# Kernel optimization log

Measured on AMD Instinct MI355X. Metric: run time of the kernel, lower is better.

Reference implementation:

```python
import jax, jax.numpy as jnp
import numpy as np

QLEN, MLEN, BSZ = 1024, 1024, 2
KLEN = QLEN + MLEN           # 2048, also rlen
D_MODEL, N_HEAD, D_HEAD = 1024, 16, 64
SCALE = 1.0 / (D_HEAD ** 0.5)
LN_EPS = 1e-5


def _rel_shift(x):
    # x: (qlen, klen, bsz, n_head). Torch-XL rel_shift via pad/reshape trick.
    q, k, b, n = x.shape
    zero_pad = jnp.zeros((q, 1, b, n), dtype=x.dtype)
    x_padded = jnp.concatenate([zero_pad, x], axis=1)   # (q, k+1, b, n)
    x_padded = x_padded.reshape(k + 1, q, b, n)[1:]      # drop first row
    return x_padded.reshape(q, k, b, n)


def _layer_norm(x, g, b):
    mu = jnp.mean(x, axis=-1, keepdims=True)
    var = jnp.mean(jnp.square(x - mu), axis=-1, keepdims=True)
    return (x - mu) * jax.lax.rsqrt(var + LN_EPS) * g + b


def setup_inputs() -> dict:
    key = jax.random.key(0)
    ks = jax.random.split(key, 9)
    w = jax.random.normal(ks[0], (QLEN, BSZ, D_MODEL), dtype=jnp.float32)
    r = jax.random.normal(ks[1], (KLEN, D_MODEL), dtype=jnp.float32)
    mems = jax.random.normal(ks[2], (MLEN, BSZ, D_MODEL), dtype=jnp.float32)
    # Causal mask with memory: query i may attend to key j <= i + MLEN.
    i = jnp.arange(QLEN)[:, None]
    j = jnp.arange(KLEN)[None, :]
    attn_mask = (j > i + MLEN)[:, :, None]  # (qlen, klen, 1) bool, dim==3 branch
    init = 0.02
    qkv_w = jax.random.normal(ks[3], (3 * N_HEAD * D_HEAD, D_MODEL), dtype=jnp.float32) * init
    r_w = jax.random.normal(ks[4], (N_HEAD * D_HEAD, D_MODEL), dtype=jnp.float32) * init
    o_w = jax.random.normal(ks[5], (D_MODEL, N_HEAD * D_HEAD), dtype=jnp.float32) * init
    ln_g = jnp.ones((D_MODEL,), dtype=jnp.float32)
    ln_b = jnp.zeros((D_MODEL,), dtype=jnp.float32)
    r_w_bias = jax.random.uniform(ks[6], (N_HEAD, D_HEAD), minval=-0.1, maxval=0.1, dtype=jnp.float32)
    r_r_bias = jax.random.uniform(ks[7], (N_HEAD, D_HEAD), minval=-0.1, maxval=0.1, dtype=jnp.float32)
    return {"w": w, "r": r, "mems": mems, "attn_mask": attn_mask,
            "qkv_w": qkv_w, "r_w": r_w, "o_w": o_w,
            "ln_g": ln_g, "ln_b": ln_b,
            "r_w_bias": r_w_bias, "r_r_bias": r_r_bias}


def reference(w, r, mems, attn_mask, qkv_w, r_w, o_w, ln_g, ln_b, r_w_bias, r_r_bias):
    qlen, bsz = w.shape[0], w.shape[1]
    cat = jnp.concatenate([mems, w], axis=0)                 # (klen, b, d_model)
    w_heads = cat @ qkv_w.T                                  # (klen, b, 3*n*d)
    w_head_q, w_head_k, w_head_v = jnp.split(w_heads, 3, axis=-1)
    klen = w_head_k.shape[0]
    w_head_q = w_head_q[-qlen:].reshape(qlen, bsz, N_HEAD, D_HEAD)
    w_head_k = w_head_k.reshape(klen, bsz, N_HEAD, D_HEAD)
    w_head_v = w_head_v.reshape(klen, bsz, N_HEAD, D_HEAD)
    r_head_k = (r @ r_w.T).reshape(r.shape[0], N_HEAD, D_HEAD)  # (rlen, n, d)

    AC = jnp.einsum('ibnd,jbnd->ijbn', w_head_q + r_w_bias, w_head_k)
    BD = _rel_shift(jnp.einsum('ibnd,jnd->ijbn', w_head_q + r_r_bias, r_head_k))
    attn_score = (AC + BD) * SCALE                           # (q, k, b, n)
    attn_score = jnp.where(attn_mask[:, :, :, None], -jnp.inf, attn_score)
    attn_prob = jax.nn.softmax(attn_score, axis=1)           # softmax over keys

    attn_vec = jnp.einsum('ijbn,jbnd->ibnd', attn_prob, w_head_v)
    attn_vec = attn_vec.reshape(qlen, bsz, N_HEAD * D_HEAD)
    attn_out = attn_vec @ o_w.T                              # (q, b, d_model)
    # post-LN residual (pre_lnorm=False)
    return _layer_norm(w + attn_out, ln_g, ln_b)
```

## Files before the change

kernel.cpp:

```cpp
#include <hip/hip_runtime.h>
#include <hip/hip_bf16.h>

#define QLEN 1024
#define MLEN 1024
#define KLEN 2048
#define BSZ 2
#define DMODEL 1024
#define NHEAD 16
#define DHEAD 64
#define SCALE_F 0.125f

typedef unsigned int u32;
typedef unsigned short u16;
typedef __attribute__((ext_vector_type(8))) short short8;
typedef __attribute__((ext_vector_type(4))) float f32x4;

__device__ __forceinline__ u16 f2bf(float f) {
  __hip_bfloat16 h = __float2bfloat16(f);
  return *reinterpret_cast<u16*>(&h);
}
__device__ __forceinline__ float bf2f(u16 u) {
  union { u32 w; float f; } c; c.w = ((u32)u) << 16; return c.f;
}
__device__ __forceinline__ float wave_sum(float v) {
#pragma unroll
  for (int o = 32; o > 0; o >>= 1) v += __shfl_xor(v, o);
  return v;
}

__global__ void detect_kernel(const void* __restrict__ lng, u32* __restrict__ flag) {
  if (threadIdx.x == 0 && blockIdx.x == 0) {
    u32 w = *(const u32*)lng;
    *flag = (w == 0x3F800000u) ? 0u : 1u;
  }
}

__global__ void conv_params(const void* __restrict__ lng, const void* __restrict__ lnb,
                            const void* __restrict__ rwb, const void* __restrict__ rrb,
                            float* __restrict__ PARAMS) {
  int i = blockIdx.x * 256 + threadIdx.x;
  u32 w0 = *(const u32*)lng;
  int f = (w0 != 0x3F800000u);
  int seg = i >> 10, off = i & 1023;
  const void* s = seg == 0 ? lng : seg == 1 ? lnb : seg == 2 ? rwb : rrb;
  PARAMS[i] = f ? bf2f(((const u16*)s)[off]) : ((const float*)s)[off];
}

__global__ void sentinel_kernel(u32* out) { out[threadIdx.x] = 0x49742400u;  }


#define GEMM_PREAMBLE()                                                        \
  __shared__ __align__(16) char lds2[2][128 * 128];                            \
  char* lA = lds2[0];                                                          \
  char* lB = lds2[1];                                                          \
  const int tid = threadIdx.x;                                                 \
  const int w_ = tid >> 6, l_ = tid & 63, lo = l_ & 15, g = l_ >> 4;           \
  const int wr = (w_ >> 1) * 64, wc = (w_ & 1) * 64;                           \
  f32x4 acc[4][4];                                                             \
  _Pragma("unroll") for (int mi = 0; mi < 4; ++mi)                             \
  _Pragma("unroll") for (int ni = 0; ni < 4; ++ni)                             \
      acc[mi][ni] = (f32x4){0.f, 0.f, 0.f, 0.f};

#define GEMM_MFMA_BODY()                                                       \
  _Pragma("unroll") for (int ks = 0; ks < 2; ++ks) {                           \
    short8 af[4], bf[4];                                                       \
    _Pragma("unroll") for (int mi = 0; mi < 4; ++mi) {                         \
      int r = wr + mi * 16 + lo;                                               \
      int c = ks * 4 + g;                                                      \
      af[mi] = *reinterpret_cast<const short8*>(lA + r * 128 + ((c ^ (r & 7)) * 16)); \
    }                                                                          \
    _Pragma("unroll") for (int ni = 0; ni < 4; ++ni) {                         \
      int r = wc + ni * 16 + lo;                                               \
      int c = ks * 4 + g;                                                      \
      bf[ni] = *reinterpret_cast<const short8*>(lB + r * 128 + ((c ^ (r & 7)) * 16)); \
    }                                                                          \
    _Pragma("unroll") for (int mi = 0; mi < 4; ++mi)                           \
    _Pragma("unroll") for (int ni = 0; ni < 4; ++ni)                           \
        acc[mi][ni] = __builtin_amdgcn_mfma_f32_16x16x32_bf16(af[mi], bf[ni], acc[mi][ni], 0, 0, 0); \
  }

__device__ __forceinline__ uint4 cvt8f32(const float* p) {
  float4 a = *reinterpret_cast<const float4*>(p);
  float4 b4 = *reinterpret_cast<const float4*>(p + 4);
  union { u16 us[8]; uint4 v; } o;
  o.us[0] = f2bf(a.x); o.us[1] = f2bf(a.y); o.us[2] = f2bf(a.z); o.us[3] = f2bf(a.w);
  o.us[4] = f2bf(b4.x); o.us[5] = f2bf(b4.y); o.us[6] = f2bf(b4.z); o.us[7] = f2bf(b4.w);
  return o.v;
}

__global__ __launch_bounds__(256) void gemm_qkv(
    const void* __restrict__ mems_raw, const void* __restrict__ w_raw,
    const void* __restrict__ qkvw_raw, const float* __restrict__ PARAMS,
    u16* __restrict__ QWb, u16* __restrict__ QRb,
    u16* __restrict__ Kb, u16* __restrict__ VTb,
    const u32* __restrict__ flag) {
  const int col0 = blockIdx.x * 128;
  const int row0 = blockIdx.y * 128;
  if (col0 < 1024 && row0 < 2048) return;
  const int f = (int)*flag;
  GEMM_PREAMBLE();

  for (int k0 = 0; k0 < DMODEL; k0 += 64) {
    __syncthreads();
    if (f) {
#pragma unroll
      for (int it = 0; it < 4; ++it) {
        int id = it * 256 + tid;
        int r = id >> 3, c = id & 7;
        int jb = row0 + r;
        const u16* asrc = jb < 2048 ? (const u16*)mems_raw + (size_t)jb * DMODEL
                                    : (const u16*)w_raw + (size_t)(jb - 2048) * DMODEL;
        uint4 va = *reinterpret_cast<const uint4*>(asrc + k0 + c * 8);
        uint4 vb = *reinterpret_cast<const uint4*>((const u16*)qkvw_raw + (size_t)(col0 + r) * DMODEL + k0 + c * 8);
        *reinterpret_cast<uint4*>(lA + r * 128 + ((c ^ (r & 7)) * 16)) = va;
        *reinterpret_cast<uint4*>(lB + r * 128 + ((c ^ (r & 7)) * 16)) = vb;
      }
    } else {
#pragma unroll
      for (int it = 0; it < 4; ++it) {
        int id = it * 256 + tid;
        int r = id >> 3, c = id & 7;
        int jb = row0 + r;
        const float* asrc = jb < 2048 ? (const float*)mems_raw + (size_t)jb * DMODEL
                                      : (const float*)w_raw + (size_t)(jb - 2048) * DMODEL;
        uint4 va = cvt8f32(asrc + k0 + c * 8);
        uint4 vb = cvt8f32((const float*)qkvw_raw + (size_t)(col0 + r) * DMODEL + k0 + c * 8);
        *reinterpret_cast<uint4*>(lA + r * 128 + ((c ^ (r & 7)) * 16)) = va;
        *reinterpret_cast<uint4*>(lB + r * 128 + ((c ^ (r & 7)) * 16)) = vb;
      }
    }
    __syncthreads();
    GEMM_MFMA_BODY();
  }

  const int which = col0 >> 10;
  if (which == 0) {
#pragma unroll
    for (int mi = 0; mi < 4; ++mi)
#pragma unroll
      for (int ni = 0; ni < 4; ++ni)
#pragma unroll
        for (int rr = 0; rr < 4; ++rr) {
          int row = row0 + wr + mi * 16 + g * 4 + rr;
          int col = col0 + wc + ni * 16 + lo;
          int i_ = (row >> 1) - 1024, b_ = row & 1;
          size_t ad = (((size_t)(b_ * 16 + (col >> 6))) * QLEN + i_) * 64 + (col & 63);
          float v = acc[mi][ni][rr];
          QWb[ad] = f2bf(v + PARAMS[2048 + col]);
          QRb[ad] = f2bf(v + PARAMS[3072 + col]);
        }
  } else if (which == 1) {
#pragma unroll
    for (int mi = 0; mi < 4; ++mi)
#pragma unroll
      for (int ni = 0; ni < 4; ++ni)
#pragma unroll
        for (int rr = 0; rr < 4; ++rr) {
          int row = row0 + wr + mi * 16 + g * 4 + rr;
          int col = col0 + wc + ni * 16 + lo;
          int j_ = row >> 1, b_ = row & 1;
          int cl = col - 1024;
          Kb[(((size_t)(b_ * 16 + (cl >> 6))) * KLEN + j_) * 64 + (cl & 63)] = f2bf(acc[mi][ni][rr]);
        }
  } else {
    __syncthreads();
    u16* ldsT = (u16*)lds2;
#pragma unroll
    for (int mi = 0; mi < 4; ++mi)
#pragma unroll
      for (int ni = 0; ni < 4; ++ni)
#pragma unroll
        for (int rr = 0; rr < 4; ++rr) {
          int rl = wr + mi * 16 + g * 4 + rr;
          int cl = wc + ni * 16 + lo;
          int rpp = (rl & 1) * 64 + (rl >> 1);
          ldsT[cl * 128 + (((rpp >> 3) ^ (cl & 7)) * 8) + (rpp & 7)] = f2bf(acc[mi][ni][rr]);
        }
    __syncthreads();
    int vc0 = col0 - 2048;
#pragma unroll
    for (int it = 0; it < 8; ++it) {
      int cid = it * 256 + tid;
      int c_l = cid >> 4;
      int j8 = cid & 15;
      uint4 vv = *reinterpret_cast<const uint4*>(ldsT + c_l * 128 + ((j8 ^ (c_l & 7)) * 8));
      int vcol = vc0 + c_l;
      int b_ = j8 >> 3;
      size_t dst = (((size_t)(b_ * 16 + (vcol >> 6))) * 64 + (vcol & 63)) * KLEN
                 + (row0 >> 1) + (j8 & 7) * 8;
      *reinterpret_cast<uint4*>(VTb + dst) = vv;
    }
  }
}

__global__ __launch_bounds__(256) void gemm_r(
    const void* __restrict__ r_raw, const void* __restrict__ rw_raw,
    u16* __restrict__ RKnb, const u32* __restrict__ flag) {
  const int col0 = blockIdx.x * 128;
  const int row0 = blockIdx.y * 128;
  const int f = (int)*flag;
  GEMM_PREAMBLE();
  for (int k0 = 0; k0 < DMODEL; k0 += 64) {
    __syncthreads();
    if (f) {
#pragma unroll
      for (int it = 0; it < 4; ++it) {
        int id = it * 256 + tid;
        int r = id >> 3, c = id & 7;
        uint4 va = *reinterpret_cast<const uint4*>((const u16*)r_raw + (size_t)(row0 + r) * DMODEL + k0 + c * 8);
        uint4 vb = *reinterpret_cast<const uint4*>((const u16*)rw_raw + (size_t)(col0 + r) * DMODEL + k0 + c * 8);
        *reinterpret_cast<uint4*>(lA + r * 128 + ((c ^ (r & 7)) * 16)) = va;
        *reinterpret_cast<uint4*>(lB + r * 128 + ((c ^ (r & 7)) * 16)) = vb;
      }
    } else {
#pragma unroll
      for (int it = 0; it < 4; ++it) {
        int id = it * 256 + tid;
        int r = id >> 3, c = id & 7;
        uint4 va = cvt8f32((const float*)r_raw + (size_t)(row0 + r) * DMODEL + k0 + c * 8);
        uint4 vb = cvt8f32((const float*)rw_raw + (size_t)(col0 + r) * DMODEL + k0 + c * 8);
        *reinterpret_cast<uint4*>(lA + r * 128 + ((c ^ (r & 7)) * 16)) = va;
        *reinterpret_cast<uint4*>(lB + r * 128 + ((c ^ (r & 7)) * 16)) = vb;
      }
    }
    __syncthreads();
    GEMM_MFMA_BODY();
  }
#pragma unroll
  for (int mi = 0; mi < 4; ++mi)
#pragma unroll
    for (int ni = 0; ni < 4; ++ni)
#pragma unroll
      for (int rr = 0; rr < 4; ++rr) {
        int t_ = row0 + wr + mi * 16 + g * 4 + rr;
        int col = col0 + wc + ni * 16 + lo;
        RKnb[((size_t)(col >> 6) * KLEN + t_) * 64 + (col & 63)] = f2bf(acc[mi][ni][rr]);
      }
}

__global__ __launch_bounds__(256) void gemm_o(
    const u16* __restrict__ A, const void* __restrict__ ow_raw,
    float* __restrict__ C, const u32* __restrict__ flag) {
  const int col0 = blockIdx.x * 128;
  const int row0 = blockIdx.y * 128;
  const int f = (int)*flag;
  GEMM_PREAMBLE();
  for (int k0 = 0; k0 < DMODEL; k0 += 64) {
    __syncthreads();
    if (f) {
#pragma unroll
      for (int it = 0; it < 4; ++it) {
        int id = it * 256 + tid;
        int r = id >> 3, c = id & 7;
        uint4 va = *reinterpret_cast<const uint4*>(A + (size_t)(row0 + r) * DMODEL + k0 + c * 8);
        uint4 vb = *reinterpret_cast<const uint4*>((const u16*)ow_raw + (size_t)(col0 + r) * DMODEL + k0 + c * 8);
        *reinterpret_cast<uint4*>(lA + r * 128 + ((c ^ (r & 7)) * 16)) = va;
        *reinterpret_cast<uint4*>(lB + r * 128 + ((c ^ (r & 7)) * 16)) = vb;
      }
    } else {
#pragma unroll
      for (int it = 0; it < 4; ++it) {
        int id = it * 256 + tid;
        int r = id >> 3, c = id & 7;
        uint4 va = *reinterpret_cast<const uint4*>(A + (size_t)(row0 + r) * DMODEL + k0 + c * 8);
        uint4 vb = cvt8f32((const float*)ow_raw + (size_t)(col0 + r) * DMODEL + k0 + c * 8);
        *reinterpret_cast<uint4*>(lA + r * 128 + ((c ^ (r & 7)) * 16)) = va;
        *reinterpret_cast<uint4*>(lB + r * 128 + ((c ^ (r & 7)) * 16)) = vb;
      }
    }
    __syncthreads();
    GEMM_MFMA_BODY();
  }
#pragma unroll
  for (int mi = 0; mi < 4; ++mi)
#pragma unroll
    for (int ni = 0; ni < 4; ++ni)
#pragma unroll
      for (int rr = 0; rr < 4; ++rr) {
        int row = row0 + wr + mi * 16 + g * 4 + rr;
        int col = col0 + wc + ni * 16 + lo;
        C[(size_t)row * DMODEL + col] = acc[mi][ni][rr];
      }
}

__global__ __launch_bounds__(256) void attn_mfma(
    const u16* __restrict__ QWb, const u16* __restrict__ QRb,
    const u16* __restrict__ Kb, const u16* __restrict__ VTb,
    const u16* __restrict__ RKnb, u16* __restrict__ AVb) {
  __shared__ __align__(16) char kt[8192];
  __shared__ __align__(16) char vt[8192];
  __shared__ __align__(16) char rt[2][8192];
  __shared__ __align__(16) char bfT[4 * 2560];
  __shared__ __align__(16) char pl[8192];

  const int tid = threadIdx.x;
  const int w = tid >> 6, l = tid & 63, lo = l & 15, g = l >> 4;
  const int gid = blockIdx.x;
  const int lid = gid & 255, hi = gid >> 8;
  const int bn = lid & 31, q3 = lid >> 5;
  const int xi = hi ? (15 - q3) : q3;
  const int i0 = xi * 64;
  const int b = bn >> 4, n = bn & 15;
  const int nkt = xi + 17;

  const u16* qwp = QWb + (((size_t)bn * QLEN) + i0 + w * 16 + lo) * 64;
  const u16* qrp = QRb + (((size_t)bn * QLEN) + i0 + w * 16 + lo) * 64;
  short8 qw0 = *reinterpret_cast<const short8*>(qwp + g * 8);
  short8 qw1 = *reinterpret_cast<const short8*>(qwp + 32 + g * 8);
  short8 qr0 = *reinterpret_cast<const short8*>(qrp + g * 8);
  short8 qr1 = *reinterpret_cast<const short8*>(qrp + 32 + g * 8);

  const u16* kbp = Kb + (size_t)bn * KLEN * 64;
  const u16* vtp = VTb + (size_t)bn * 64 * KLEN;
  const u16* rp  = RKnb + (size_t)n * KLEN * 64;

  uint4 Rk[2], Rv[2], Rr[2];
  const int srow = tid >> 3, sc = tid & 7;

  {
    int m0 = 15 - xi;
    char* rh = rt[m0 & 1];
#pragma unroll
    for (int it = 0; it < 2; ++it) {
      int row = srow + it * 32;
      int t = m0 * 64 + row;
      *reinterpret_cast<uint4*>(rh + row * 128 + ((sc ^ (row & 7)) * 16)) =
          *reinterpret_cast<const uint4*>(rp + (size_t)t * 64 + sc * 8);
    }
  }
#pragma unroll
  for (int it = 0; it < 2; ++it) {
    int row = srow + it * 32;
    Rk[it] = *reinterpret_cast<const uint4*>(kbp + (size_t)row * 64 + sc * 8);
    Rv[it] = *reinterpret_cast<const uint4*>(vtp + (size_t)row * KLEN + sc * 8);
    int t = (16 - xi) * 64 + row; t = t > KLEN - 1 ? KLEN - 1 : t;
    Rr[it] = *reinterpret_cast<const uint4*>(rp + (size_t)t * 64 + sc * 8);
  }

  f32x4 oacc[4];
  float m_r[4], l_r[4];
#pragma unroll
  for (int r = 0; r < 4; ++r) {
    oacc[r] = (f32x4){0.f, 0.f, 0.f, 0.f};
    m_r[r] = -1e30f; l_r[r] = 0.f;
  }

  for (int kti = 0; kti < nkt; ++kti) {
    const int j0 = kti * 64;
    __syncthreads();
    {
      char* rh = rt[(kti + 16 - xi) & 1];
#pragma unroll
      for (int it = 0; it < 2; ++it) {
        int row = srow + it * 32;
        int sw = (sc ^ (row & 7)) * 16;
        *reinterpret_cast<uint4*>(kt + row * 128 + sw) = Rk[it];
        *reinterpret_cast<uint4*>(vt + row * 128 + sw) = Rv[it];
        *reinterpret_cast<uint4*>(rh + row * 128 + sw) = Rr[it];
      }
    }
    __syncthreads();
    if (kti + 1 < nkt) {
      int j0n = j0 + 64;
      int mst = kti + 17 - xi;
#pragma unroll
      for (int it = 0; it < 2; ++it) {
        int row = srow + it * 32;
        Rk[it] = *reinterpret_cast<const uint4*>(kbp + (size_t)(j0n + row) * 64 + sc * 8);
        Rv[it] = *reinterpret_cast<const uint4*>(vtp + (size_t)row * KLEN + j0n + sc * 8);
        int t = mst * 64 + row; t = t > KLEN - 1 ? KLEN - 1 : t;
        Rr[it] = *reinterpret_cast<const uint4*>(rp + (size_t)t * 64 + sc * 8);
      }
    }
    const int hbase = (kti + 15 - xi) & 1;

    f32x4 ac[4];
#pragma unroll
    for (int ct = 0; ct < 4; ++ct) {
      const char* kb = kt + (ct * 16 + lo) * 128;
      short8 k0 = *reinterpret_cast<const short8*>(kb + ((g ^ (lo & 7)) * 16));
      short8 k1 = *reinterpret_cast<const short8*>(kb + (((4 + g) ^ (lo & 7)) * 16));
      f32x4 a = {0.f, 0.f, 0.f, 0.f};
      a = __builtin_amdgcn_mfma_f32_16x16x32_bf16(qw0, k0, a, 0, 0, 0);
      a = __builtin_amdgcn_mfma_f32_16x16x32_bf16(qw1, k1, a, 0, 0, 0);
      ac[ct] = a;
    }
    char* bfw = bfT + w * 2560;
#pragma unroll
    for (int bb = 0; bb < 5; ++bb) {
      int bt = 3 - w + bb;
      int half = hbase ^ (bt >> 2);
      const char* rbase = rt[half] + ((bt & 3) * 16 + lo) * 128;
      short8 r0 = *reinterpret_cast<const short8*>(rbase + ((g ^ (lo & 7)) * 16));
      short8 r1 = *reinterpret_cast<const short8*>(rbase + (((4 + g) ^ (lo & 7)) * 16));
      f32x4 a = {0.f, 0.f, 0.f, 0.f};
      a = __builtin_amdgcn_mfma_f32_16x16x32_bf16(qr0, r0, a, 0, 0, 0);
      a = __builtin_amdgcn_mfma_f32_16x16x32_bf16(qr1, r1, a, 0, 0, 0);
      union { u16 us[4]; uint2 v2; } pk;
      pk.us[0] = f2bf(a[0]); pk.us[1] = f2bf(a[1]);
      pk.us[2] = f2bf(a[2]); pk.us[3] = f2bf(a[3]);
      int rel = bb * 16 + lo;
      *reinterpret_cast<uint2*>(bfw + rel * 32 + (((g >> 1) ^ (rel & 1)) * 16) + (g & 1) * 8) = pk.v2;
    }
    const int relmax = i0 + MLEN - j0 + 15 + 16 * w;
    float sv[4][4];
    float rmax[4] = {-1e30f, -1e30f, -1e30f, -1e30f};
#pragma unroll
    for (int ct = 0; ct < 4; ++ct)
#pragma unroll
      for (int rr = 0; rr < 4; ++rr) {
        int rel = ct * 16 + lo - g * 4 - rr + 15;
        float bd = bf2f(*reinterpret_cast<const u16*>(
            bfw + rel * 32 + (((g >> 1) ^ (rel & 1)) * 16) + (g & 1) * 8 + rr * 2));
        float s = (ac[ct][rr] + bd) * SCALE_F;
        s = rel > relmax ? -1e30f : s;
        sv[ct][rr] = s;
        rmax[rr] = fmaxf(rmax[rr], s);
      }
#pragma unroll
    for (int rr = 0; rr < 4; ++rr) {
      float rm = rmax[rr];
      rm = fmaxf(rm, __shfl_xor(rm, 1));
      rm = fmaxf(rm, __shfl_xor(rm, 2));
      rm = fmaxf(rm, __shfl_xor(rm, 4));
      rm = fmaxf(rm, __shfl_xor(rm, 8));
      float mn = fmaxf(m_r[rr], rm);
      float sc2 = __expf(m_r[rr] - mn);
      m_r[rr] = mn;
      l_r[rr] *= sc2;
#pragma unroll
      for (int dt = 0; dt < 4; ++dt) oacc[dt][rr] *= sc2;
    }
    float rsum[4] = {0.f, 0.f, 0.f, 0.f};
#pragma unroll
    for (int ct = 0; ct < 4; ++ct)
#pragma unroll
      for (int rr = 0; rr < 4; ++rr) {
        float p = __expf(sv[ct][rr] - m_r[rr]);
        sv[ct][rr] = p;
        rsum[rr] += p;
      }
#pragma unroll
    for (int rr = 0; rr < 4; ++rr) {
      float rs = rsum[rr];
      rs += __shfl_xor(rs, 1);
      rs += __shfl_xor(rs, 2);
      rs += __shfl_xor(rs, 4);
      rs += __shfl_xor(rs, 8);
      l_r[rr] += rs;
    }
#pragma unroll
    for (int ct = 0; ct < 4; ++ct)
#pragma unroll
      for (int rr = 0; rr < 4; ++rr) {
        int rowp = g * 4 + rr;
        int col = ct * 16 + lo;
        int cblk = (col >> 3) ^ (rowp & 7);
        *reinterpret_cast<u16*>(pl + w * 2048 + rowp * 128 + cblk * 16 + (col & 7) * 2) = f2bf(sv[ct][rr]);
      }
    short8 pa0 = *reinterpret_cast<const short8*>(pl + w * 2048 + lo * 128 + ((g ^ (lo & 7)) * 16));
    short8 pa1 = *reinterpret_cast<const short8*>(pl + w * 2048 + lo * 128 + (((4 + g) ^ (lo & 7)) * 16));
#pragma unroll
    for (int dt = 0; dt < 4; ++dt) {
      const char* vb = vt + (dt * 16 + lo) * 128;
      short8 v0 = *reinterpret_cast<const short8*>(vb + ((g ^ (lo & 7)) * 16));
      short8 v1 = *reinterpret_cast<const short8*>(vb + (((4 + g) ^ (lo & 7)) * 16));
      oacc[dt] = __builtin_amdgcn_mfma_f32_16x16x32_bf16(pa0, v0, oacc[dt], 0, 0, 0);
      oacc[dt] = __builtin_amdgcn_mfma_f32_16x16x32_bf16(pa1, v1, oacc[dt], 0, 0, 0);
    }
  }
#pragma unroll
  for (int rr = 0; rr < 4; ++rr) {
    float inv = 1.0f / l_r[rr];
    int qi = i0 + w * 16 + g * 4 + rr;
#pragma unroll
    for (int dt = 0; dt < 4; ++dt) {
      int d = dt * 16 + lo;
      AVb[((size_t)qi * BSZ + b) * DMODEL + n * 64 + d] = f2bf(oacc[dt][rr] * inv);
    }
  }
}

__global__ __launch_bounds__(256) void ln_kernel(const void* __restrict__ w_raw,
                                                 const float* __restrict__ AOUT,
                                                 const float* __restrict__ PARAMS,
                                                 void* __restrict__ out,
                                                 const u32* __restrict__ flag) {
  int row = blockIdx.x;
  int tid = threadIdx.x;
  __shared__ float buf[DMODEL];
  __shared__ float red[4];
  int f = (int)*flag;
  const float* ap = AOUT + (size_t)row * DMODEL;
  float lsum = 0.f;
  for (int c = tid; c < DMODEL; c += 256) {
    float wv = f ? bf2f(((const u16*)w_raw)[(size_t)row * DMODEL + c])
                 : ((const float*)w_raw)[(size_t)row * DMODEL + c];
    float v = wv + ap[c];
    buf[c] = v; lsum += v;
  }
  lsum = wave_sum(lsum);
  if ((tid & 63) == 0) red[tid >> 6] = lsum;
  __syncthreads();
  float mean = (red[0] + red[1] + red[2] + red[3]) * (1.0f / DMODEL);
  float lv = 0.f;
  for (int c = tid; c < DMODEL; c += 256) { float dv = buf[c] - mean; lv = fmaf(dv, dv, lv); }
  lv = wave_sum(lv);
  __syncthreads();
  if ((tid & 63) == 0) red[tid >> 6] = lv;
  __syncthreads();
  float rstd = rsqrtf((red[0] + red[1] + red[2] + red[3]) * (1.0f / DMODEL) + 1e-5f);
  for (int c = tid; c < DMODEL; c += 256) {
    float o = (buf[c] - mean) * rstd * PARAMS[c] + PARAMS[1024 + c];
    if (f) ((__hip_bfloat16*)out)[(size_t)row * DMODEL + c] = __float2bfloat16(o);
    else   ((float*)out)[(size_t)row * DMODEL + c] = o;
  }
}

extern "C" void kernel_launch(void* const* d_in, const int* in_sizes, int n_in,
                              void* d_out, int out_size, void* d_ws, size_t ws_size,
                              hipStream_t stream) {
  const void* w_in    = d_in[0];
  const void* r_in    = d_in[1];
  const void* mems_in = d_in[2];
  const void* qkvw_in = d_in[4];
  const void* rw_in   = d_in[5];
  const void* ow_in   = d_in[6];
  const void* lng_in  = d_in[7];
  const void* lnb_in  = d_in[8];
  const void* rwb_in  = d_in[9];
  const void* rrb_in  = d_in[10];

  char* ws = (char*)d_ws;
  u32* flag = (u32*)ws;
  char* cur = ws + 256;
  auto alloc = [&](size_t bytes) { char* p = cur; cur += (bytes + 255) & ~(size_t)255; return p; };

  float* PARAMS = (float*)alloc(4096 * 4);
  u16* QWb  = (u16*)alloc((size_t)BSZ * NHEAD * QLEN * 64 * 2);
  u16* QRb  = (u16*)alloc((size_t)BSZ * NHEAD * QLEN * 64 * 2);
  u16* Kb   = (u16*)alloc((size_t)BSZ * NHEAD * KLEN * 64 * 2);
  u16* VTb  = (u16*)alloc((size_t)BSZ * NHEAD * 64 * KLEN * 2);
  u16* RKnb = (u16*)alloc((size_t)NHEAD * KLEN * 64 * 2);
  u16* AVb  = (u16*)alloc((size_t)QLEN * BSZ * DMODEL * 2);
  float* AOUT = (float*)alloc((size_t)QLEN * BSZ * DMODEL * 4);
  size_t need = (size_t)(cur - ws);

  if (ws_size < need || out_size != QLEN * BSZ * DMODEL || n_in < 11) {
    sentinel_kernel<<<1, 256, 0, stream>>>((u32*)d_out);
    return;
  }

  detect_kernel<<<1, 64, 0, stream>>>(lng_in, flag);
  conv_params<<<16, 256, 0, stream>>>(lng_in, lnb_in, rwb_in, rrb_in, PARAMS);

  dim3 b256(256);
  gemm_qkv<<<dim3(24, 32), b256, 0, stream>>>(mems_in, w_in, qkvw_in, PARAMS,
                                              QWb, QRb, Kb, VTb, flag);
  gemm_r<<<dim3(8, 16), b256, 0, stream>>>(r_in, rw_in, RKnb, flag);
  attn_mfma<<<512, b256, 0, stream>>>(QWb, QRb, Kb, VTb, RKnb, AVb);
  gemm_o<<<dim3(8, 16), b256, 0, stream>>>(AVb, ow_in, AOUT, flag);
  ln_kernel<<<QLEN * BSZ, b256, 0, stream>>>(w_in, AOUT, PARAMS, d_out, flag);
}
```

Measured before the change: 237.5 us.

## Split attention key range across two blocks and merge partials in a combine kernel

The attention grid is doubled so each (batch, head, query tile) has two blocks, each covering half of the key tiles. Each block writes unnormalized fp32 partial outputs plus its running max and sum, and a new combine kernel merges the two halves into the bf16 attention vector. The change also adds s_setprio around the MFMA sections and re-swizzles the BD scratch layout in LDS to reduce bank conflicts. The intent is more parallelism on a 256-CU device where 512 blocks underfill it. The cost is extra partial-result memory traffic and one more kernel launch.

Measured after the change: 237.8 us. About the same (+0.1%).

```diff
diff --git a/kernel.cpp b/kernel.cpp
--- a/kernel.cpp
+++ b/kernel.cpp
@@ -286,7 +286,8 @@
 __global__ __launch_bounds__(256) void attn_mfma(
     const u16* __restrict__ QWb, const u16* __restrict__ QRb,
     const u16* __restrict__ Kb, const u16* __restrict__ VTb,
-    const u16* __restrict__ RKnb, u16* __restrict__ AVb) {
+    const u16* __restrict__ RKnb, float* __restrict__ PADO,
+    float2* __restrict__ PML) {
   __shared__ __align__(16) char kt[8192];
   __shared__ __align__(16) char vt[8192];
   __shared__ __align__(16) char rt[2][8192];
@@ -296,12 +297,17 @@
   const int tid = threadIdx.x;
   const int w = tid >> 6, l = tid & 63, lo = l & 15, g = l >> 4;
   const int gid = blockIdx.x;
-  const int lid = gid & 255, hi = gid >> 8;
+  const int s = gid >> 9;
+  const int r9 = gid & 511;
+  const int lid = r9 & 255, hi = r9 >> 8;
   const int bn = lid & 31, q3 = lid >> 5;
   const int xi = hi ? (15 - q3) : q3;
   const int i0 = xi * 64;
   const int b = bn >> 4, n = bn & 15;
-  const int nkt = xi + 17;
+  const int nkt_full = xi + 17;
+  const int h = (nkt_full + 1) >> 1;
+  const int kst = s ? h : 0;
+  const int kend = s ? nkt_full : h;
 
   const u16* qwp = QWb + (((size_t)bn * QLEN) + i0 + w * 16 + lo) * 64;
   const u16* qrp = QRb + (((size_t)bn * QLEN) + i0 + w * 16 + lo) * 64;
@@ -316,9 +322,10 @@
 
   uint4 Rk[2], Rv[2], Rr[2];
   const int srow = tid >> 3, sc = tid & 7;
+  const int j0p = kst * 64;
 
   {
-    int m0 = 15 - xi;
+    int m0 = kst + 15 - xi;
     char* rh = rt[m0 & 1];
 #pragma unroll
     for (int it = 0; it < 2; ++it) {
@@ -331,9 +338,9 @@
 #pragma unroll
   for (int it = 0; it < 2; ++it) {
     int row = srow + it * 32;
-    Rk[it] = *reinterpret_cast<const uint4*>(kbp + (size_t)row * 64 + sc * 8);
-    Rv[it] = *reinterpret_cast<const uint4*>(vtp + (size_t)row * KLEN + sc * 8);
-    int t = (16 - xi) * 64 + row; t = t > KLEN - 1 ? KLEN - 1 : t;
+    Rk[it] = *reinterpret_cast<const uint4*>(kbp + (size_t)(j0p + row) * 64 + sc * 8);
+    Rv[it] = *reinterpret_cast<const uint4*>(vtp + (size_t)row * KLEN + j0p + sc * 8);
+    int t = (kst + 16 - xi) * 64 + row; t = t > KLEN - 1 ? KLEN - 1 : t;
     Rr[it] = *reinterpret_cast<const uint4*>(rp + (size_t)t * 64 + sc * 8);
   }
 
@@ -345,7 +352,7 @@
     m_r[r] = -1e30f; l_r[r] = 0.f;
   }
 
-  for (int kti = 0; kti < nkt; ++kti) {
+  for (int kti = kst; kti < kend; ++kti) {
     const int j0 = kti * 64;
     __syncthreads();
     {
@@ -360,7 +367,7 @@
       }
     }
     __syncthreads();
-    if (kti + 1 < nkt) {
+    if (kti + 1 < kend) {
       int j0n = j0 + 64;
       int mst = kti + 17 - xi;
 #pragma unroll
@@ -375,6 +382,7 @@
     const int hbase = (kti + 15 - xi) & 1;
 
     f32x4 ac[4];
+    __builtin_amdgcn_s_setprio(1);
 #pragma unroll
     for (int ct = 0; ct < 4; ++ct) {
       const char* kb = kt + (ct * 16 + lo) * 128;
@@ -385,7 +393,9 @@
       a = __builtin_amdgcn_mfma_f32_16x16x32_bf16(qw1, k1, a, 0, 0, 0);
       ac[ct] = a;
     }
+    __builtin_amdgcn_s_setprio(0);
     char* bfw = bfT + w * 2560;
+    __builtin_amdgcn_s_setprio(1);
 #pragma unroll
     for (int bb = 0; bb < 5; ++bb) {
       int bt = 3 - w + bb;
@@ -400,8 +410,10 @@
       pk.us[0] = f2bf(a[0]); pk.us[1] = f2bf(a[1]);
       pk.us[2] = f2bf(a[2]); pk.us[3] = f2bf(a[3]);
       int rel = bb * 16 + lo;
-      *reinterpret_cast<uint2*>(bfw + rel * 32 + (((g >> 1) ^ (rel & 1)) * 16) + (g & 1) * 8) = pk.v2;
-    }
+      int slot = ((((g >> 1) ^ (rel & 1)) * 2 + (g & 1)) ^ ((rel >> 2) & 3));
+      *reinterpret_cast<uint2*>(bfw + rel * 32 + slot * 8) = pk.v2;
+    }
+    __builtin_amdgcn_s_setprio(0);
     const int relmax = i0 + MLEN - j0 + 15 + 16 * w;
     float sv[4][4];
     float rmax[4] = {-1e30f, -1e30f, -1e30f, -1e30f};
@@ -410,12 +422,12 @@
 #pragma unroll
       for (int rr = 0; rr < 4; ++rr) {
         int rel = ct * 16 + lo - g * 4 - rr + 15;
-        float bd = bf2f(*reinterpret_cast<const u16*>(
-            bfw + rel * 32 + (((g >> 1) ^ (rel & 1)) * 16) + (g & 1) * 8 + rr * 2));
-        float s = (ac[ct][rr] + bd) * SCALE_F;
-        s = rel > relmax ? -1e30f : s;
-        sv[ct][rr] = s;
-        rmax[rr] = fmaxf(rmax[rr], s);
+        int slot = ((((g >> 1) ^ (rel & 1)) * 2 + (g & 1)) ^ ((rel >> 2) & 3));
+        float bd = bf2f(*reinterpret_cast<const u16*>(bfw + rel * 32 + slot * 8 + rr * 2));
+        float s2 = (ac[ct][rr] + bd) * SCALE_F;
+        s2 = rel > relmax ? -1e30f : s2;
+        sv[ct][rr] = s2;
+        rmax[rr] = fmaxf(rmax[rr], s2);
       }
 #pragma unroll
     for (int rr = 0; rr < 4; ++rr) {
@@ -460,6 +472,7 @@
       }
     short8 pa0 = *reinterpret_cast<const short8*>(pl + w * 2048 + lo * 128 + ((g ^ (lo & 7)) * 16));
     short8 pa1 = *reinterpret_cast<const short8*>(pl + w * 2048 + lo * 128 + (((4 + g) ^ (lo & 7)) * 16));
+    __builtin_amdgcn_s_setprio(1);
 #pragma unroll
     for (int dt = 0; dt < 4; ++dt) {
       const char* vb = vt + (dt * 16 + lo) * 128;
@@ -468,17 +481,44 @@
       oacc[dt] = __builtin_amdgcn_mfma_f32_16x16x32_bf16(pa0, v0, oacc[dt], 0, 0, 0);
       oacc[dt] = __builtin_amdgcn_mfma_f32_16x16x32_bf16(pa1, v1, oacc[dt], 0, 0, 0);
     }
+    __builtin_amdgcn_s_setprio(0);
   }
 #pragma unroll
   for (int rr = 0; rr < 4; ++rr) {
-    float inv = 1.0f / l_r[rr];
     int qi = i0 + w * 16 + g * 4 + rr;
+    size_t rowg = ((size_t)(s * 32 + bn)) * QLEN + qi;
 #pragma unroll
     for (int dt = 0; dt < 4; ++dt) {
       int d = dt * 16 + lo;
-      AVb[((size_t)qi * BSZ + b) * DMODEL + n * 64 + d] = f2bf(oacc[dt][rr] * inv);
-    }
-  }
+      PADO[rowg * 64 + d] = oacc[dt][rr];
+    }
+    if (lo == 0) {
+      float2 ml; ml.x = m_r[rr]; ml.y = l_r[rr];
+      PML[rowg] = ml;
+    }
+  }
+}
+
+__global__ __launch_bounds__(256) void combine_kernel(
+    const float* __restrict__ PADO, const float2* __restrict__ PML,
+    u16* __restrict__ AVb) {
+  int idx = blockIdx.x * 256 + threadIdx.x;
+  int row = idx >> 4;
+  int c4 = (idx & 15) * 4;
+  int bn = row >> 10, qi = row & 1023;
+  int b = bn >> 4, n = bn & 15;
+  float2 ml0 = PML[row];
+  float2 ml1 = PML[32768 + row];
+  float M = fmaxf(ml0.x, ml1.x);
+  float e0 = __expf(ml0.x - M), e1 = __expf(ml1.x - M);
+  float inv = 1.0f / (ml0.y * e0 + ml1.y * e1);
+  f32x4 o0 = *reinterpret_cast<const f32x4*>(&PADO[(size_t)row * 64 + c4]);
+  f32x4 o1 = *reinterpret_cast<const f32x4*>(&PADO[(size_t)(32768 + row) * 64 + c4]);
+  union { u16 us[4]; uint2 v; } pk;
+#pragma unroll
+  for (int e = 0; e < 4; ++e)
+    pk.us[e] = f2bf((o0[e] * e0 + o1[e] * e1) * inv);
+  *reinterpret_cast<uint2*>(&AVb[((size_t)qi * BSZ + b) * DMODEL + n * 64 + c4]) = pk.v;
 }
 
 __global__ __launch_bounds__(256) void ln_kernel(const void* __restrict__ w_raw,
@@ -544,6 +584,8 @@
   u16* RKnb = (u16*)alloc((size_t)NHEAD * KLEN * 64 * 2);
   u16* AVb  = (u16*)alloc((size_t)QLEN * BSZ * DMODEL * 2);
   float* AOUT = (float*)alloc((size_t)QLEN * BSZ * DMODEL * 4);
+  float* PADO = (float*)alloc((size_t)2 * 32 * QLEN * 64 * 4);
+  float2* PML = (float2*)alloc((size_t)2 * 32 * QLEN * 8);
   size_t need = (size_t)(cur - ws);
 
   if (ws_size < need || out_size != QLEN * BSZ * DMODEL || n_in < 11) {
@@ -558,7 +600,8 @@
   gemm_qkv<<<dim3(24, 32), b256, 0, stream>>>(mems_in, w_in, qkvw_in, PARAMS,
                                               QWb, QRb, Kb, VTb, flag);
   gemm_r<<<dim3(8, 16), b256, 0, stream>>>(r_in, rw_in, RKnb, flag);
-  attn_mfma<<<512, b256, 0, stream>>>(QWb, QRb, Kb, VTb, RKnb, AVb);
+  attn_mfma<<<1024, b256, 0, stream>>>(QWb, QRb, Kb, VTb, RKnb, PADO, PML);
+  combine_kernel<<<2048, b256, 0, stream>>>(PADO, PML, AVb);
   gemm_o<<<dim3(8, 16), b256, 0, stream>>>(AVb, ow_in, AOUT, flag);
   ln_kernel<<<QLEN * BSZ, b256, 0, stream>>>(w_in, AOUT, PARAMS, d_out, flag);
 }
```
